# Optimization experiments

Hardware: AMD Instinct MI355X
Metric: run time of the kernel (lower is better)

## Reference

```python
import jax, jax.numpy as jnp
import numpy as np

N_NODES = 50000
N_EDGES = 800000
F_IN = 128
HEADS = 4
HEAD_DIM = 32  # hidden_size // heads
HIDDEN = HEADS * HEAD_DIM
N_GRAPHS = 64
LEAKY_SLOPE = 0.01
EPS_LN = 1e-5


def setup_inputs() -> dict:
    key = jax.random.key(0)
    ks = jax.random.split(key, 12)
    x = jax.random.normal(ks[0], (N_NODES, F_IN), dtype=jnp.float32)
    edge_index = jax.random.randint(ks[1], (2, N_EDGES), 0, N_NODES, dtype=jnp.int64)
    batch = jnp.sort(jax.random.randint(ks[2], (N_NODES,), 0, N_GRAPHS, dtype=jnp.int64))
    s = 1.0 / np.sqrt(F_IN).astype(np.float32)
    Wq = jax.random.normal(ks[3], (F_IN, HIDDEN), dtype=jnp.float32) * s
    bq = jnp.zeros((HIDDEN,), jnp.float32)
    Wk = jax.random.normal(ks[4], (F_IN, HIDDEN), dtype=jnp.float32) * s
    bk = jnp.zeros((HIDDEN,), jnp.float32)
    Wv = jax.random.normal(ks[5], (F_IN, HIDDEN), dtype=jnp.float32) * s
    bv = jnp.zeros((HIDDEN,), jnp.float32)
    Ws = jax.random.normal(ks[6], (F_IN, HIDDEN), dtype=jnp.float32) * s  # root/skip lin
    bs = jnp.zeros((HIDDEN,), jnp.float32)
    ln_w = jnp.ones((HIDDEN,), jnp.float32)
    ln_b = jnp.zeros((HIDDEN,), jnp.float32)
    return {"x": x, "edge_index": edge_index, "batch": batch,
            "Wq": Wq, "bq": bq, "Wk": Wk, "bk": bk, "Wv": Wv, "bv": bv,
            "Ws": Ws, "bs": bs, "ln_w": ln_w, "ln_b": ln_b}


def reference(x, edge_index, batch, Wq, bq, Wk, bk, Wv, bv, Ws, bs, ln_w, ln_b):
    N = x.shape[0]
    src, dst = edge_index[0], edge_index[1]  # message j(src) -> i(dst)
    q = (x @ Wq + bq).reshape(N, HEADS, HEAD_DIM)
    k = (x @ Wk + bk).reshape(N, HEADS, HEAD_DIM)
    v = (x @ Wv + bv).reshape(N, HEADS, HEAD_DIM)
    # per-edge attention logits [E, H]
    alpha = jnp.einsum('ehc,ehc->eh', q[dst], k[src]) / jnp.sqrt(jnp.float32(HEAD_DIM))
    # scatter-softmax over incoming edges of each destination node
    m = jax.ops.segment_max(alpha, dst, num_segments=N)
    m = jnp.where(jnp.isfinite(m), m, 0.0)  # empty segments -> -inf; neutralize
    ex = jnp.exp(alpha - m[dst])
    denom = jax.ops.segment_sum(ex, dst, num_segments=N)
    attn = ex / (denom[dst] + 1e-16)
    # scatter-add aggregation of weighted values, concat heads
    out = jax.ops.segment_sum(attn[:, :, None] * v[src], dst, num_segments=N)
    out = out.reshape(N, HIDDEN) + x @ Ws + bs  # root/skip connection
    # PyG graph-mode LayerNorm: normalize over all nodes+channels of each graph
    cnt = jax.ops.segment_sum(jnp.ones((N,), out.dtype), batch, num_segments=N_GRAPHS)
    norm = jnp.maximum(cnt, 1.0) * HIDDEN
    mean = jax.ops.segment_sum(out.sum(-1), batch, num_segments=N_GRAPHS) / norm
    outc = out - mean[batch][:, None]
    var = jax.ops.segment_sum((outc * outc).sum(-1), batch, num_segments=N_GRAPHS) / norm
    y = outc / jnp.sqrt(var + EPS_LN)[batch][:, None]
    y = y * ln_w + ln_b
    y = jnp.where(y > 0, y, LEAKY_SLOPE * y)  # LeakyReLU
    return (y, attn)
```

## Files before the change

kernel.cpp:

```cpp
#include <hip/hip_runtime.h>
#include <hip/hip_fp16.h>

constexpr int N_NODES = 50000;
constexpr int N_EDGES = 800000;
constexpr int HIDDEN  = 128;
constexpr float RSQRT_D = 0.17677669529663687f;
constexpr int Y_SIZE = N_NODES * HIDDEN;
constexpr int M_PAD  = 50048;
constexpr int SCAN_BLOCKS = 196;

constexpr size_t OFF_Q      = 0;
constexpr size_t OFF_K      = 6400000;
constexpr size_t OFF_V      = 12800000;
constexpr size_t OFF_S      = 19200000;
constexpr size_t OFF_DENOM  = 25600000;
constexpr size_t OFF_GSUM   = 25800000;
constexpr size_t OFF_GVAR   = 25800064;
constexpr size_t OFF_GCNT   = 25800128;
constexpr size_t OFF_DEG    = 25800192;
constexpr size_t OFF_OFFS   = 25850192;
constexpr size_t OFF_CURSOR = 25900224;
constexpr size_t OFF_CSRSRC = 25950224;
constexpr size_t OFF_CSREID = 26750224;
constexpr size_t OFF_PART   = 27550224;

typedef __attribute__((ext_vector_type(8))) short bf16x8;
typedef __attribute__((ext_vector_type(4))) float f32x4;

__device__ __forceinline__ short f2bf(float f) {
    unsigned u = __float_as_uint(f);
    unsigned r = (u + 0x7fff + ((u >> 16) & 1)) >> 16;
    return (short)r;
}

__device__ __forceinline__ void gload_lds16(const void* g, void* l) {
    __builtin_amdgcn_global_load_lds(
        (const __attribute__((address_space(1))) void*)g,
        (__attribute__((address_space(3))) void*)l, 16, 0, 0);
}

__global__ __launch_bounds__(256) void k_cvt_x(const float* __restrict__ x,
                                               short* __restrict__ xs)
{
    int tid = blockIdx.x * 256 + threadIdx.x;
    int row = tid >> 4, ci = tid & 15;
    short o[8];
    if (row < N_NODES) {
        float4 a = *(const float4*)&x[(size_t)row * 128 + ci * 8];
        float4 b = *(const float4*)&x[(size_t)row * 128 + ci * 8 + 4];
        o[0] = f2bf(a.x); o[1] = f2bf(a.y); o[2] = f2bf(a.z); o[3] = f2bf(a.w);
        o[4] = f2bf(b.x); o[5] = f2bf(b.y); o[6] = f2bf(b.z); o[7] = f2bf(b.w);
    } else {
        #pragma unroll
        for (int j = 0; j < 8; ++j) o[j] = 0;
    }
    int cs = ci ^ (row & 7);
    *(int4*)&xs[(size_t)row * 128 + cs * 8] = *(int4*)o;
}

__global__ __launch_bounds__(256) void k_cvt_w(
    const float* __restrict__ Wq, const float* __restrict__ Wk,
    const float* __restrict__ Wv, const float* __restrict__ Wsm,
    short* __restrict__ wt)
{
    int tid = blockIdx.x * 256 + threadIdx.x;
    int mat = tid >> 11, n = (tid >> 4) & 127, kg = tid & 15;
    const float* W = (mat == 0) ? Wq : (mat == 1) ? Wk : (mat == 2) ? Wv : Wsm;
    short o[8];
    #pragma unroll
    for (int j = 0; j < 8; ++j) o[j] = f2bf(W[(kg * 8 + j) * 128 + n]);
    int cs = kg ^ (n & 7);
    *(int4*)&wt[mat * 16384 + n * 128 + cs * 8] = *(int4*)o;
}

__global__ __launch_bounds__(256) void k_mm(
    const short* __restrict__ xs, const short* __restrict__ wt,
    const float* __restrict__ bq, const float* __restrict__ bk,
    const float* __restrict__ bv, const float* __restrict__ bs,
    float* __restrict__ q, __half* __restrict__ kb,
    __half* __restrict__ vb, float* __restrict__ s)
{
    __shared__ __align__(16) char As[32768];
    __shared__ __align__(16) char Bs[32768];
    const int t = threadIdx.x, lane = t & 63, wv = t >> 6;
    const int bm = blockIdx.x >> 2, nt = blockIdx.x & 3;
    const int m0 = bm * 128;

    const char* gA = (const char*)xs + (size_t)m0 * 256;
    const char* gB = (const char*)wt + nt * 32768;
    #pragma unroll
    for (int i = 0; i < 8; ++i) {
        int chunk = wv * 8 + i;
        gload_lds16(gA + chunk * 1024 + lane * 16, As + chunk * 1024);
        gload_lds16(gB + chunk * 1024 + lane * 16, Bs + chunk * 1024);
    }

    const float* Bb = (nt == 0) ? bq : (nt == 1) ? bk : (nt == 2) ? bv : bs;
    const int wm = wv >> 1, wn = wv & 1;
    f32x4 acc[4][4];
    #pragma unroll
    for (int nf = 0; nf < 4; ++nf) {
        float bc = Bb[wn * 64 + nf * 16 + (lane & 15)];
        #pragma unroll
        for (int mf = 0; mf < 4; ++mf) acc[mf][nf] = (f32x4){bc, bc, bc, bc};
    }
    __syncthreads();

    #pragma unroll
    for (int ks = 0; ks < 4; ++ks) {
        bf16x8 af[4], bfr[4];
        const int cbase = ks * 64 + ((lane >> 4) << 4);
        #pragma unroll
        for (int mf = 0; mf < 4; ++mf) {
            int mr = wm * 64 + mf * 16 + (lane & 15);
            af[mf] = *(const bf16x8*)(As + mr * 256 + (cbase ^ ((mr & 7) << 4)));
        }
        #pragma unroll
        for (int nf = 0; nf < 4; ++nf) {
            int nc = wn * 64 + nf * 16 + (lane & 15);
            bfr[nf] = *(const bf16x8*)(Bs + nc * 256 + (cbase ^ ((nc & 7) << 4)));
        }
        #pragma unroll
        for (int mf = 0; mf < 4; ++mf)
            #pragma unroll
            for (int nf = 0; nf < 4; ++nf)
                acc[mf][nf] = __builtin_amdgcn_mfma_f32_16x16x32_bf16(
                    af[mf], bfr[nf], acc[mf][nf], 0, 0, 0);
    }

    const int colbase = wn * 64 + (lane & 15);
    if (nt == 0 || nt == 3) {
        float* O = (nt == 0) ? q : s;
        #pragma unroll
        for (int mf = 0; mf < 4; ++mf) {
            int rowb = m0 + wm * 64 + mf * 16 + ((lane >> 4) << 2);
            #pragma unroll
            for (int nf = 0; nf < 4; ++nf) {
                int col = colbase + nf * 16;
                #pragma unroll
                for (int r = 0; r < 4; ++r) {
                    int node = rowb + r;
                    if (node < N_NODES) O[(size_t)node * 128 + col] = acc[mf][nf][r];
                }
            }
        }
    } else {
        __half* O = (nt == 1) ? kb : vb;
        #pragma unroll
        for (int mf = 0; mf < 4; ++mf) {
            int rowb = m0 + wm * 64 + mf * 16 + ((lane >> 4) << 2);
            #pragma unroll
            for (int nf = 0; nf < 4; ++nf) {
                int col = colbase + nf * 16;
                #pragma unroll
                for (int r = 0; r < 4; ++r) {
                    int node = rowb + r;
                    if (node < N_NODES)
                        O[(size_t)node * 128 + col] = __float2half_rn(acc[mf][nf][r]);
                }
            }
        }
    }
}

__global__ __launch_bounds__(256) void k_hist(const int* __restrict__ dst,
                                              int* __restrict__ deg)
{
    int e = blockIdx.x * 256 + threadIdx.x;
    atomicAdd(&deg[dst[e]], 1);
}

__global__ __launch_bounds__(256) void k_scan1(const int* __restrict__ deg,
                                               int* __restrict__ part)
{
    const int t = threadIdx.x;
    int idx = blockIdx.x * 256 + t;
    int v = (idx < N_NODES) ? deg[idx] : 0;
    #pragma unroll
    for (int o = 1; o < 64; o <<= 1) v += __shfl_xor(v, o);
    __shared__ int wsum[4];
    if ((t & 63) == 0) wsum[t >> 6] = v;
    __syncthreads();
    if (t == 0) part[blockIdx.x] = wsum[0] + wsum[1] + wsum[2] + wsum[3];
}

__global__ __launch_bounds__(256) void k_scan2(int* __restrict__ part)
{
    __shared__ int buf[256];
    const int t = threadIdx.x;
    int v = (t < SCAN_BLOCKS) ? part[t] : 0;
    buf[t] = v;
    __syncthreads();
    for (int o = 1; o < 256; o <<= 1) {
        int tmp = (t >= o) ? buf[t - o] : 0;
        __syncthreads();
        buf[t] += tmp;
        __syncthreads();
    }
    if (t < SCAN_BLOCKS) part[t] = buf[t] - v;
}

__global__ __launch_bounds__(256) void k_scan3(const int* __restrict__ deg,
                                               const int* __restrict__ part,
                                               int* __restrict__ offs,
                                               int* __restrict__ cursor)
{
    const int t = threadIdx.x;
    const int idx = blockIdx.x * 256 + t;
    const int lane = t & 63, w = t >> 6;
    int v = (idx < N_NODES) ? deg[idx] : 0;
    int inc = v;
    #pragma unroll
    for (int o = 1; o < 64; o <<= 1) {
        int nb = __shfl_up(inc, o);
        if (lane >= o) inc += nb;
    }
    __shared__ int wsum[4];
    if (lane == 63) wsum[w] = inc;
    __syncthreads();
    int wbase = 0;
    #pragma unroll
    for (int i = 0; i < 4; ++i) if (i < w) wbase += wsum[i];
    int excl = part[blockIdx.x] + wbase + inc - v;
    if (idx < N_NODES) {
        offs[idx] = excl;
        cursor[idx] = excl;
    }
    if (idx == 0) offs[N_NODES] = N_EDGES;
}

__global__ __launch_bounds__(256) void k_scatter(
    const int* __restrict__ src, const int* __restrict__ dst,
    int* __restrict__ cursor, int* __restrict__ csr_src, int* __restrict__ csr_eid)
{
    int e = blockIdx.x * 256 + threadIdx.x;
    int d = dst[e];
    int pos = atomicAdd(&cursor[d], 1);
    csr_src[pos] = src[e];
    csr_eid[pos] = e;
}

__global__ __launch_bounds__(256) void k_fused(
    const float* __restrict__ q, const __half2* __restrict__ kb,
    const __half2* __restrict__ vb, const float* __restrict__ s,
    const int* __restrict__ offs, const int* __restrict__ csr_src,
    const int* __restrict__ csr_eid,
    float* __restrict__ exbuf, float* __restrict__ denom,
    float* __restrict__ outb)
{
    const int t = threadIdx.x;
    const int lane = t & 63;
    const int n = blockIdx.x * 4 + (t >> 6);
    const int begin = offs[n], end = offs[n + 1];
    const float2 qv = *(const float2*)&q[(size_t)n * 128 + lane * 2];
    const int h = lane >> 4;
    float acc0 = 0.f, acc1 = 0.f, dsum = 0.f;
    int i = begin;
    for (; i + 4 <= end; i += 4) {
        int sn[4], eid[4];
        #pragma unroll
        for (int u = 0; u < 4; ++u) { sn[u] = csr_src[i + u]; eid[u] = csr_eid[i + u]; }
        __half2 kh[4], vh[4];
        #pragma unroll
        for (int u = 0; u < 4; ++u) kh[u] = kb[(size_t)sn[u] * 64 + lane];
        #pragma unroll
        for (int u = 0; u < 4; ++u) vh[u] = vb[(size_t)sn[u] * 64 + lane];
        float p[4];
        #pragma unroll
        for (int u = 0; u < 4; ++u) {
            float2 kf = __half22float2(kh[u]);
            p[u] = qv.x * kf.x + qv.y * kf.y;
        }
        #pragma unroll
        for (int u = 0; u < 4; ++u) p[u] += __shfl_xor(p[u], 1);
        #pragma unroll
        for (int u = 0; u < 4; ++u) p[u] += __shfl_xor(p[u], 2);
        #pragma unroll
        for (int u = 0; u < 4; ++u) p[u] += __shfl_xor(p[u], 4);
        #pragma unroll
        for (int u = 0; u < 4; ++u) p[u] += __shfl_xor(p[u], 8);
        #pragma unroll
        for (int u = 0; u < 4; ++u) {
            float ex = __expf(p[u] * RSQRT_D);
            dsum += ex;
            float2 vf = __half22float2(vh[u]);
            acc0 += ex * vf.x;
            acc1 += ex * vf.y;
            if ((lane & 15) == 0) exbuf[eid[u] * 4 + h] = ex;
        }
    }
    for (; i < end; ++i) {
        const int sn0 = csr_src[i];
        const int e0  = csr_eid[i];
        const __half2 kh0 = kb[(size_t)sn0 * 64 + lane];
        const __half2 vh0 = vb[(size_t)sn0 * 64 + lane];
        const float2 k0 = __half22float2(kh0);
        float p0 = qv.x * k0.x + qv.y * k0.y;
        p0 += __shfl_xor(p0, 1);
        p0 += __shfl_xor(p0, 2);
        p0 += __shfl_xor(p0, 4);
        p0 += __shfl_xor(p0, 8);
        const float ex0 = __expf(p0 * RSQRT_D);
        dsum += ex0;
        const float2 v0 = __half22float2(vh0);
        acc0 += ex0 * v0.x;
        acc1 += ex0 * v0.y;
        if ((lane & 15) == 0) exbuf[e0 * 4 + h] = ex0;
    }
    if ((lane & 15) == 0) denom[n * 4 + h] = dsum;
    const float rdn = 1.f / (dsum + 1e-16f);
    const float2 sv = *(const float2*)&s[(size_t)n * 128 + lane * 2];
    float2 o = make_float2(acc0 * rdn + sv.x, acc1 * rdn + sv.y);
    *(float2*)&outb[(size_t)n * 128 + lane * 2] = o;
}

__global__ __launch_bounds__(256) void k_norm(
    float* __restrict__ attn, const float* __restrict__ denom,
    const int* __restrict__ dst)
{
    int idx = blockIdx.x * 256 + threadIdx.x;
    int e = idx >> 2, h = idx & 3;
    attn[idx] = attn[idx] / (denom[dst[e] * 4 + h] + 1e-16f);
}

__global__ __launch_bounds__(256) void k_sum(
    const float* __restrict__ out, const int* __restrict__ batch,
    float* __restrict__ gsum, int* __restrict__ gcnt)
{
    __shared__ float nsum[32];
    __shared__ int   ngr[32];
    const int t = threadIdx.x;
    const int nl = t >> 3, part = t & 7;
    const int n = blockIdx.x * 32 + nl;
    float lsum = 0.f;
    if (n < N_NODES) {
        size_t base = (size_t)n * 128 + part * 16;
        #pragma unroll
        for (int i = 0; i < 4; ++i) {
            float4 o = *(const float4*)&out[base + i * 4];
            lsum += o.x + o.y + o.z + o.w;
        }
    }
    lsum += __shfl_xor(lsum, 1);
    lsum += __shfl_xor(lsum, 2);
    lsum += __shfl_xor(lsum, 4);
    if (part == 0) { nsum[nl] = lsum; ngr[nl] = (n < N_NODES) ? batch[n] : -1; }
    __syncthreads();
    if (t == 0) {
        float acc = 0.f; int cg = ngr[0], cnt = 0;
        for (int i = 0; i < 32; ++i) {
            int g = ngr[i];
            if (g != cg) {
                if (cg >= 0) { atomicAdd(&gsum[cg], acc); atomicAdd(&gcnt[cg], cnt); }
                acc = 0.f; cnt = 0; cg = g;
            }
            acc += nsum[i]; ++cnt;
        }
        if (cg >= 0) { atomicAdd(&gsum[cg], acc); atomicAdd(&gcnt[cg], cnt); }
    }
}

__global__ __launch_bounds__(256) void k_var(
    const float* __restrict__ out, const int* __restrict__ batch,
    const float* __restrict__ gsum, const int* __restrict__ gcnt,
    float* __restrict__ gvar)
{
    __shared__ float nsum[32];
    __shared__ int   ngr[32];
    const int t = threadIdx.x;
    const int nl = t >> 3, part = t & 7;
    const int n = blockIdx.x * 32 + nl;
    float lsum = 0.f;
    if (n < N_NODES) {
        int g = batch[n];
        float mean = gsum[g] / (fmaxf((float)gcnt[g], 1.f) * 128.f);
        size_t base = (size_t)n * 128 + part * 16;
        #pragma unroll
        for (int i = 0; i < 4; ++i) {
            float4 o = *(const float4*)&out[base + i * 4];
            float dx = o.x - mean, dy = o.y - mean, dz = o.z - mean, dw = o.w - mean;
            lsum += dx * dx + dy * dy + dz * dz + dw * dw;
        }
    }
    lsum += __shfl_xor(lsum, 1);
    lsum += __shfl_xor(lsum, 2);
    lsum += __shfl_xor(lsum, 4);
    if (part == 0) { nsum[nl] = lsum; ngr[nl] = (n < N_NODES) ? batch[n] : -1; }
    __syncthreads();
    if (t == 0) {
        float acc = 0.f; int cg = ngr[0];
        for (int i = 0; i < 32; ++i) {
            int g = ngr[i];
            if (g != cg) {
                if (cg >= 0) atomicAdd(&gvar[cg], acc);
                acc = 0.f; cg = g;
            }
            acc += nsum[i];
        }
        if (cg >= 0) atomicAdd(&gvar[cg], acc);
    }
}

__global__ __launch_bounds__(256) void k_final(
    const float* __restrict__ out, const int* __restrict__ batch,
    const float* __restrict__ gsum, const float* __restrict__ gvar,
    const int* __restrict__ gcnt,
    const float* __restrict__ lnw, const float* __restrict__ lnb,
    float* __restrict__ y)
{
    int idx = blockIdx.x * 256 + threadIdx.x;
    int n = idx >> 7, c = idx & 127;
    int g = batch[n];
    float norm = fmaxf((float)gcnt[g], 1.f) * 128.f;
    float mean = gsum[g] / norm;
    float var  = gvar[g] / norm;
    float inv  = rsqrtf(var + 1e-5f);
    float val  = (out[idx] - mean) * inv * lnw[c] + lnb[c];
    y[idx] = val > 0.f ? val : 0.01f * val;
}

extern "C" void kernel_launch(void* const* d_in, const int* in_sizes, int n_in,
                              void* d_out, int out_size, void* d_ws, size_t ws_size,
                              hipStream_t stream)
{
    (void)in_sizes; (void)n_in; (void)out_size; (void)ws_size;
    const float* x    = (const float*)d_in[0];
    const int*   ei   = (const int*)  d_in[1];
    const int*   batch= (const int*)  d_in[2];
    const float* Wq   = (const float*)d_in[3];
    const float* bq   = (const float*)d_in[4];
    const float* Wk   = (const float*)d_in[5];
    const float* bk   = (const float*)d_in[6];
    const float* Wv   = (const float*)d_in[7];
    const float* bv   = (const float*)d_in[8];
    const float* Wsm  = (const float*)d_in[9];
    const float* bs   = (const float*)d_in[10];
    const float* lnw  = (const float*)d_in[11];
    const float* lnb  = (const float*)d_in[12];

    float* outp = (float*)d_out;
    float* ws   = (float*)d_ws;

    const int* srcI = ei;
    const int* dstI = ei + N_EDGES;

    float*  q       = ws + OFF_Q;
    __half* kb      = (__half*)(ws + OFF_K);
    __half* vb      = (__half*)(ws + OFF_V);
    float*  s       = ws + OFF_S;
    float*  denom   = ws + OFF_DENOM;
    short*  wt      = (short*)(ws + OFF_DENOM);
    float*  gsum    = ws + OFF_GSUM;
    float*  gvar    = ws + OFF_GVAR;
    int*    gcnt    = (int*)(ws + OFF_GCNT);
    int*    deg     = (int*)(ws + OFF_DEG);
    int*    offs    = (int*)(ws + OFF_OFFS);
    int*    cursor  = (int*)(ws + OFF_CURSOR);
    int*    csr_src = (int*)(ws + OFF_CSRSRC);
    int*    csr_eid = (int*)(ws + OFF_CSREID);
    int*    partArr = (int*)(ws + OFF_PART);

    float* outb  = outp;
    short* x_swz = (short*)outp;
    float* attn  = outp + Y_SIZE;

    hipMemsetAsync(gsum, 0, (size_t)(192 + N_NODES) * sizeof(float), stream);

    k_cvt_w<<<32, 256, 0, stream>>>(Wq, Wk, Wv, Wsm, wt);
    k_cvt_x<<<(M_PAD * 16) / 256, 256, 0, stream>>>(x, x_swz);
    k_mm<<<(M_PAD / 128) * 4, 256, 0, stream>>>(x_swz, wt, bq, bk, bv, bs,
                                                q, kb, vb, s);

    k_hist<<<N_EDGES / 256, 256, 0, stream>>>(dstI, deg);
    k_scan1<<<SCAN_BLOCKS, 256, 0, stream>>>(deg, partArr);
    k_scan2<<<1, 256, 0, stream>>>(partArr);
    k_scan3<<<SCAN_BLOCKS, 256, 0, stream>>>(deg, partArr, offs, cursor);
    k_scatter<<<N_EDGES / 256, 256, 0, stream>>>(srcI, dstI, cursor, csr_src, csr_eid);
    k_fused<<<N_NODES / 4, 256, 0, stream>>>(q, (const __half2*)kb, (const __half2*)vb,
                                             s, offs, csr_src, csr_eid,
                                             attn, denom, outb);
    k_norm<<<(N_EDGES * 4) / 256, 256, 0, stream>>>(attn, denom, dstI);
    k_sum<<<(N_NODES + 31) / 32, 256, 0, stream>>>(outb, batch, gsum, gcnt);
    k_var<<<(N_NODES + 31) / 32, 256, 0, stream>>>(outb, batch, gsum, gcnt, gvar);
    k_final<<<Y_SIZE / 256, 256, 0, stream>>>(outb, batch, gsum, gvar, gcnt,
                                              lnw, lnb, outp);
}
```

Before: 272.6 us.

## Fuse conversions, compute all projections per tile, pack CSR, single-pass LN stats

Merges the x and W conversion kernels into one launch. The GEMM now loads each A tile once and loops over all four weight matrices, reloading B into shared memory between them, and q is stored as fp16. CSR source and edge-id arrays become one interleaved int2 array, and the gather loop is unrolled to 8 edges. The separate sum and variance passes are replaced by one pass that accumulates sum and sum of squares, computing variance as E[x^2]-mean^2, which risks cancellation error.

```diff
diff --git a/kernel.cpp b/kernel.cpp
--- a/kernel.cpp
+++ b/kernel.cpp
@@ -8,6 +8,7 @@
 constexpr int Y_SIZE = N_NODES * HIDDEN;
 constexpr int M_PAD  = 50048;
 constexpr int SCAN_BLOCKS = 196;
+constexpr int XCVT_BLOCKS = (M_PAD * 16) / 256;
 
 constexpr size_t OFF_Q      = 0;
 constexpr size_t OFF_K      = 6400000;
@@ -15,13 +16,12 @@
 constexpr size_t OFF_S      = 19200000;
 constexpr size_t OFF_DENOM  = 25600000;
 constexpr size_t OFF_GSUM   = 25800000;
-constexpr size_t OFF_GVAR   = 25800064;
+constexpr size_t OFF_GSQ    = 25800064;
 constexpr size_t OFF_GCNT   = 25800128;
 constexpr size_t OFF_DEG    = 25800192;
 constexpr size_t OFF_OFFS   = 25850192;
 constexpr size_t OFF_CURSOR = 25900224;
-constexpr size_t OFF_CSRSRC = 25950224;
-constexpr size_t OFF_CSREID = 26750224;
+constexpr size_t OFF_CSR    = 25950224;
 constexpr size_t OFF_PART   = 27550224;
 
 typedef __attribute__((ext_vector_type(8))) short bf16x8;
@@ -39,127 +39,141 @@
         (__attribute__((address_space(3))) void*)l, 16, 0, 0);
 }
 
-__global__ __launch_bounds__(256) void k_cvt_x(const float* __restrict__ x,
-                                               short* __restrict__ xs)
-{
-    int tid = blockIdx.x * 256 + threadIdx.x;
-    int row = tid >> 4, ci = tid & 15;
-    short o[8];
-    if (row < N_NODES) {
-        float4 a = *(const float4*)&x[(size_t)row * 128 + ci * 8];
-        float4 b = *(const float4*)&x[(size_t)row * 128 + ci * 8 + 4];
-        o[0] = f2bf(a.x); o[1] = f2bf(a.y); o[2] = f2bf(a.z); o[3] = f2bf(a.w);
-        o[4] = f2bf(b.x); o[5] = f2bf(b.y); o[6] = f2bf(b.z); o[7] = f2bf(b.w);
-    } else {
-        #pragma unroll
-        for (int j = 0; j < 8; ++j) o[j] = 0;
-    }
-    int cs = ci ^ (row & 7);
-    *(int4*)&xs[(size_t)row * 128 + cs * 8] = *(int4*)o;
-}
-
-__global__ __launch_bounds__(256) void k_cvt_w(
+__global__ __launch_bounds__(256) void k_cvt(
+    const float* __restrict__ x,
     const float* __restrict__ Wq, const float* __restrict__ Wk,
     const float* __restrict__ Wv, const float* __restrict__ Wsm,
-    short* __restrict__ wt)
-{
-    int tid = blockIdx.x * 256 + threadIdx.x;
-    int mat = tid >> 11, n = (tid >> 4) & 127, kg = tid & 15;
-    const float* W = (mat == 0) ? Wq : (mat == 1) ? Wk : (mat == 2) ? Wv : Wsm;
-    short o[8];
-    #pragma unroll
-    for (int j = 0; j < 8; ++j) o[j] = f2bf(W[(kg * 8 + j) * 128 + n]);
-    int cs = kg ^ (n & 7);
-    *(int4*)&wt[mat * 16384 + n * 128 + cs * 8] = *(int4*)o;
+    short* __restrict__ xs, short* __restrict__ wt)
+{
+    int b = blockIdx.x;
+    if (b < XCVT_BLOCKS) {
+        int tid = b * 256 + threadIdx.x;
+        int row = tid >> 4, ci = tid & 15;
+        short o[8];
+        if (row < N_NODES) {
+            float4 a = *(const float4*)&x[(size_t)row * 128 + ci * 8];
+            float4 bb = *(const float4*)&x[(size_t)row * 128 + ci * 8 + 4];
+            o[0] = f2bf(a.x); o[1] = f2bf(a.y); o[2] = f2bf(a.z); o[3] = f2bf(a.w);
+            o[4] = f2bf(bb.x); o[5] = f2bf(bb.y); o[6] = f2bf(bb.z); o[7] = f2bf(bb.w);
+        } else {
+            #pragma unroll
+            for (int j = 0; j < 8; ++j) o[j] = 0;
+        }
+        int cs = ci ^ (row & 7);
+        *(int4*)&xs[(size_t)row * 128 + cs * 8] = *(int4*)o;
+    } else {
+        int tid = (b - XCVT_BLOCKS) * 256 + threadIdx.x;
+        int mat = tid >> 11, n = (tid >> 4) & 127, kg = tid & 15;
+        const float* W = (mat == 0) ? Wq : (mat == 1) ? Wk : (mat == 2) ? Wv : Wsm;
+        short o[8];
+        #pragma unroll
+        for (int j = 0; j < 8; ++j) o[j] = f2bf(W[(kg * 8 + j) * 128 + n]);
+        int cs = kg ^ (n & 7);
+        *(int4*)&wt[mat * 16384 + n * 128 + cs * 8] = *(int4*)o;
+    }
 }
 
 __global__ __launch_bounds__(256) void k_mm(
     const short* __restrict__ xs, const short* __restrict__ wt,
     const float* __restrict__ bq, const float* __restrict__ bk,
     const float* __restrict__ bv, const float* __restrict__ bs,
-    float* __restrict__ q, __half* __restrict__ kb,
+    __half* __restrict__ q, __half* __restrict__ kb,
     __half* __restrict__ vb, float* __restrict__ s)
 {
     __shared__ __align__(16) char As[32768];
     __shared__ __align__(16) char Bs[32768];
     const int t = threadIdx.x, lane = t & 63, wv = t >> 6;
-    const int bm = blockIdx.x >> 2, nt = blockIdx.x & 3;
-    const int m0 = bm * 128;
+    const int m0 = blockIdx.x * 128;
+    const int wm = wv >> 1, wn = wv & 1;
 
     const char* gA = (const char*)xs + (size_t)m0 * 256;
-    const char* gB = (const char*)wt + nt * 32768;
     #pragma unroll
     for (int i = 0; i < 8; ++i) {
         int chunk = wv * 8 + i;
         gload_lds16(gA + chunk * 1024 + lane * 16, As + chunk * 1024);
-        gload_lds16(gB + chunk * 1024 + lane * 16, Bs + chunk * 1024);
-    }
-
-    const float* Bb = (nt == 0) ? bq : (nt == 1) ? bk : (nt == 2) ? bv : bs;
-    const int wm = wv >> 1, wn = wv & 1;
-    f32x4 acc[4][4];
-    #pragma unroll
-    for (int nf = 0; nf < 4; ++nf) {
-        float bc = Bb[wn * 64 + nf * 16 + (lane & 15)];
-        #pragma unroll
-        for (int mf = 0; mf < 4; ++mf) acc[mf][nf] = (f32x4){bc, bc, bc, bc};
+        gload_lds16((const char*)wt + chunk * 1024 + lane * 16, Bs + chunk * 1024);
     }
     __syncthreads();
 
+    bf16x8 af[4][4];
     #pragma unroll
     for (int ks = 0; ks < 4; ++ks) {
-        bf16x8 af[4], bfr[4];
         const int cbase = ks * 64 + ((lane >> 4) << 4);
         #pragma unroll
         for (int mf = 0; mf < 4; ++mf) {
             int mr = wm * 64 + mf * 16 + (lane & 15);
-            af[mf] = *(const bf16x8*)(As + mr * 256 + (cbase ^ ((mr & 7) << 4)));
-        }
+            af[ks][mf] = *(const bf16x8*)(As + mr * 256 + (cbase ^ ((mr & 7) << 4)));
+        }
+    }
+
+    const float* Bbs[4] = {bq, bk, bv, bs};
+    #pragma unroll
+    for (int mat = 0; mat < 4; ++mat) {
+        f32x4 acc[4][4];
         #pragma unroll
         for (int nf = 0; nf < 4; ++nf) {
-            int nc = wn * 64 + nf * 16 + (lane & 15);
-            bfr[nf] = *(const bf16x8*)(Bs + nc * 256 + (cbase ^ ((nc & 7) << 4)));
-        }
-        #pragma unroll
-        for (int mf = 0; mf < 4; ++mf)
-            #pragma unroll
-            for (int nf = 0; nf < 4; ++nf)
-                acc[mf][nf] = __builtin_amdgcn_mfma_f32_16x16x32_bf16(
-                    af[mf], bfr[nf], acc[mf][nf], 0, 0, 0);
-    }
-
-    const int colbase = wn * 64 + (lane & 15);
-    if (nt == 0 || nt == 3) {
-        float* O = (nt == 0) ? q : s;
-        #pragma unroll
-        for (int mf = 0; mf < 4; ++mf) {
-            int rowb = m0 + wm * 64 + mf * 16 + ((lane >> 4) << 2);
+            float bc = Bbs[mat][wn * 64 + nf * 16 + (lane & 15)];
+            #pragma unroll
+            for (int mf = 0; mf < 4; ++mf) acc[mf][nf] = (f32x4){bc, bc, bc, bc};
+        }
+        #pragma unroll
+        for (int ks = 0; ks < 4; ++ks) {
+            bf16x8 bfr[4];
+            const int cbase = ks * 64 + ((lane >> 4) << 4);
             #pragma unroll
             for (int nf = 0; nf < 4; ++nf) {
-                int col = colbase + nf * 16;
+                int nc = wn * 64 + nf * 16 + (lane & 15);
+                bfr[nf] = *(const bf16x8*)(Bs + nc * 256 + (cbase ^ ((nc & 7) << 4)));
+            }
+            #pragma unroll
+            for (int mf = 0; mf < 4; ++mf)
                 #pragma unroll
-                for (int r = 0; r < 4; ++r) {
-                    int node = rowb + r;
-                    if (node < N_NODES) O[(size_t)node * 128 + col] = acc[mf][nf][r];
+                for (int nf = 0; nf < 4; ++nf)
+                    acc[mf][nf] = __builtin_amdgcn_mfma_f32_16x16x32_bf16(
+                        af[ks][mf], bfr[nf], acc[mf][nf], 0, 0, 0);
+        }
+        __syncthreads();
+        if (mat < 3) {
+            const char* gB = (const char*)wt + (mat + 1) * 32768;
+            #pragma unroll
+            for (int i = 0; i < 8; ++i) {
+                int chunk = wv * 8 + i;
+                gload_lds16(gB + chunk * 1024 + lane * 16, Bs + chunk * 1024);
+            }
+        }
+        const int colbase = wn * 64 + (lane & 15);
+        if (mat == 3) {
+            #pragma unroll
+            for (int mf = 0; mf < 4; ++mf) {
+                int rowb = m0 + wm * 64 + mf * 16 + ((lane >> 4) << 2);
+                #pragma unroll
+                for (int nf = 0; nf < 4; ++nf) {
+                    int col = colbase + nf * 16;
+                    #pragma unroll
+                    for (int r = 0; r < 4; ++r) {
+                        int node = rowb + r;
+                        if (node < N_NODES) s[(size_t)node * 128 + col] = acc[mf][nf][r];
+                    }
                 }
             }
-        }
-    } else {
-        __half* O = (nt == 1) ? kb : vb;
-        #pragma unroll
-        for (int mf = 0; mf < 4; ++mf) {
-            int rowb = m0 + wm * 64 + mf * 16 + ((lane >> 4) << 2);
-            #pragma unroll
-            for (int nf = 0; nf < 4; ++nf) {
-                int col = colbase + nf * 16;
+        } else {
+            __half* O = (mat == 0) ? q : (mat == 1) ? kb : vb;
+            #pragma unroll
+            for (int mf = 0; mf < 4; ++mf) {
+                int rowb = m0 + wm * 64 + mf * 16 + ((lane >> 4) << 2);
                 #pragma unroll
-                for (int r = 0; r < 4; ++r) {
-                    int node = rowb + r;
-                    if (node < N_NODES)
-                        O[(size_t)node * 128 + col] = __float2half_rn(acc[mf][nf][r]);
+                for (int nf = 0; nf < 4; ++nf) {
+                    int col = colbase + nf * 16;
+                    #pragma unroll
+                    for (int r = 0; r < 4; ++r) {
+                        int node = rowb + r;
+                        if (node < N_NODES)
+                            O[(size_t)node * 128 + col] = __float2half_rn(acc[mf][nf][r]);
+                    }
                 }
             }
         }
+        __syncthreads();
     }
 }
 
@@ -231,20 +245,18 @@
 
 __global__ __launch_bounds__(256) void k_scatter(
     const int* __restrict__ src, const int* __restrict__ dst,
-    int* __restrict__ cursor, int* __restrict__ csr_src, int* __restrict__ csr_eid)
+    int* __restrict__ cursor, int2* __restrict__ csr)
 {
     int e = blockIdx.x * 256 + threadIdx.x;
     int d = dst[e];
     int pos = atomicAdd(&cursor[d], 1);
-    csr_src[pos] = src[e];
-    csr_eid[pos] = e;
+    csr[pos] = make_int2(src[e], e);
 }
 
 __global__ __launch_bounds__(256) void k_fused(
-    const float* __restrict__ q, const __half2* __restrict__ kb,
+    const __half2* __restrict__ qb, const __half2* __restrict__ kb,
     const __half2* __restrict__ vb, const float* __restrict__ s,
-    const int* __restrict__ offs, const int* __restrict__ csr_src,
-    const int* __restrict__ csr_eid,
+    const int* __restrict__ offs, const int2* __restrict__ csr,
     float* __restrict__ exbuf, float* __restrict__ denom,
     float* __restrict__ outb)
 {
@@ -252,48 +264,48 @@
     const int lane = t & 63;
     const int n = blockIdx.x * 4 + (t >> 6);
     const int begin = offs[n], end = offs[n + 1];
-    const float2 qv = *(const float2*)&q[(size_t)n * 128 + lane * 2];
+    const float2 qv = __half22float2(qb[(size_t)n * 64 + lane]);
+    const float2 sv = *(const float2*)&s[(size_t)n * 128 + lane * 2];
     const int h = lane >> 4;
     float acc0 = 0.f, acc1 = 0.f, dsum = 0.f;
     int i = begin;
-    for (; i + 4 <= end; i += 4) {
-        int sn[4], eid[4];
-        #pragma unroll
-        for (int u = 0; u < 4; ++u) { sn[u] = csr_src[i + u]; eid[u] = csr_eid[i + u]; }
-        __half2 kh[4], vh[4];
-        #pragma unroll
-        for (int u = 0; u < 4; ++u) kh[u] = kb[(size_t)sn[u] * 64 + lane];
-        #pragma unroll
-        for (int u = 0; u < 4; ++u) vh[u] = vb[(size_t)sn[u] * 64 + lane];
-        float p[4];
-        #pragma unroll
-        for (int u = 0; u < 4; ++u) {
+    for (; i + 8 <= end; i += 8) {
+        int2 c[8];
+        #pragma unroll
+        for (int u = 0; u < 8; ++u) c[u] = csr[i + u];
+        __half2 kh[8], vh[8];
+        #pragma unroll
+        for (int u = 0; u < 8; ++u) kh[u] = kb[(size_t)c[u].x * 64 + lane];
+        #pragma unroll
+        for (int u = 0; u < 8; ++u) vh[u] = vb[(size_t)c[u].x * 64 + lane];
+        float p[8];
+        #pragma unroll
+        for (int u = 0; u < 8; ++u) {
             float2 kf = __half22float2(kh[u]);
             p[u] = qv.x * kf.x + qv.y * kf.y;
         }
         #pragma unroll
-        for (int u = 0; u < 4; ++u) p[u] += __shfl_xor(p[u], 1);
-        #pragma unroll
-        for (int u = 0; u < 4; ++u) p[u] += __shfl_xor(p[u], 2);
-        #pragma unroll
-        for (int u = 0; u < 4; ++u) p[u] += __shfl_xor(p[u], 4);
-        #pragma unroll
-        for (int u = 0; u < 4; ++u) p[u] += __shfl_xor(p[u], 8);
-        #pragma unroll
-        for (int u = 0; u < 4; ++u) {
+        for (int u = 0; u < 8; ++u) p[u] += __shfl_xor(p[u], 1);
+        #pragma unroll
+        for (int u = 0; u < 8; ++u) p[u] += __shfl_xor(p[u], 2);
+        #pragma unroll
+        for (int u = 0; u < 8; ++u) p[u] += __shfl_xor(p[u], 4);
+        #pragma unroll
+        for (int u = 0; u < 8; ++u) p[u] += __shfl_xor(p[u], 8);
+        #pragma unroll
+        for (int u = 0; u < 8; ++u) {
             float ex = __expf(p[u] * RSQRT_D);
             dsum += ex;
             float2 vf = __half22float2(vh[u]);
             acc0 += ex * vf.x;
             acc1 += ex * vf.y;
-            if ((lane & 15) == 0) exbuf[eid[u] * 4 + h] = ex;
+            if ((lane & 15) == 0) exbuf[c[u].y * 4 + h] = ex;
         }
     }
     for (; i < end; ++i) {
-        const int sn0 = csr_src[i];
-        const int e0  = csr_eid[i];
-        const __half2 kh0 = kb[(size_t)sn0 * 64 + lane];
-        const __half2 vh0 = vb[(size_t)sn0 * 64 + lane];
+        const int2 c0 = csr[i];
+        const __half2 kh0 = kb[(size_t)c0.x * 64 + lane];
+        const __half2 vh0 = vb[(size_t)c0.x * 64 + lane];
         const float2 k0 = __half22float2(kh0);
         float p0 = qv.x * k0.x + qv.y * k0.y;
         p0 += __shfl_xor(p0, 1);
@@ -305,11 +317,10 @@
         const float2 v0 = __half22float2(vh0);
         acc0 += ex0 * v0.x;
         acc1 += ex0 * v0.y;
-        if ((lane & 15) == 0) exbuf[e0 * 4 + h] = ex0;
+        if ((lane & 15) == 0) exbuf[c0.y * 4 + h] = ex0;
     }
     if ((lane & 15) == 0) denom[n * 4 + h] = dsum;
     const float rdn = 1.f / (dsum + 1e-16f);
-    const float2 sv = *(const float2*)&s[(size_t)n * 128 + lane * 2];
     float2 o = make_float2(acc0 * rdn + sv.x, acc1 * rdn + sv.y);
     *(float2*)&outb[(size_t)n * 128 + lane * 2] = o;
 }
@@ -323,87 +334,51 @@
     attn[idx] = attn[idx] / (denom[dst[e] * 4 + h] + 1e-16f);
 }
 
-__global__ __launch_bounds__(256) void k_sum(
+__global__ __launch_bounds__(256) void k_stats(
     const float* __restrict__ out, const int* __restrict__ batch,
-    float* __restrict__ gsum, int* __restrict__ gcnt)
-{
-    __shared__ float nsum[32];
+    float* __restrict__ gsum, float* __restrict__ gsq, int* __restrict__ gcnt)
+{
+    __shared__ float nsum[32], nsq[32];
     __shared__ int   ngr[32];
     const int t = threadIdx.x;
     const int nl = t >> 3, part = t & 7;
     const int n = blockIdx.x * 32 + nl;
-    float lsum = 0.f;
+    float lsum = 0.f, lsq = 0.f;
     if (n < N_NODES) {
         size_t base = (size_t)n * 128 + part * 16;
         #pragma unroll
         for (int i = 0; i < 4; ++i) {
             float4 o = *(const float4*)&out[base + i * 4];
             lsum += o.x + o.y + o.z + o.w;
-        }
-    }
-    lsum += __shfl_xor(lsum, 1);
-    lsum += __shfl_xor(lsum, 2);
-    lsum += __shfl_xor(lsum, 4);
-    if (part == 0) { nsum[nl] = lsum; ngr[nl] = (n < N_NODES) ? batch[n] : -1; }
+            lsq  += o.x * o.x + o.y * o.y + o.z * o.z + o.w * o.w;
+        }
+    }
+    #pragma unroll
+    for (int o = 1; o < 8; o <<= 1) {
+        lsum += __shfl_xor(lsum, o);
+        lsq  += __shfl_xor(lsq, o);
+    }
+    if (part == 0) { nsum[nl] = lsum; nsq[nl] = lsq; ngr[nl] = (n < N_NODES) ? batch[n] : -1; }
     __syncthreads();
     if (t == 0) {
-        float acc = 0.f; int cg = ngr[0], cnt = 0;
+        float acc = 0.f, accq = 0.f; int cg = ngr[0], cnt = 0;
         for (int i = 0; i < 32; ++i) {
             int g = ngr[i];
             if (g != cg) {
-                if (cg >= 0) { atomicAdd(&gsum[cg], acc); atomicAdd(&gcnt[cg], cnt); }
-                acc = 0.f; cnt = 0; cg = g;
+                if (cg >= 0) { atomicAdd(&gsum[cg], acc); atomicAdd(&gsq[cg], accq);
+                               atomicAdd(&gcnt[cg], cnt); }
+                acc = 0.f; accq = 0.f; cnt = 0; cg = g;
             }
-            acc += nsum[i]; ++cnt;
-        }
-        if (cg >= 0) { atomicAdd(&gsum[cg], acc); atomicAdd(&gcnt[cg], cnt); }
-    }
-}
-
-__global__ __launch_bounds__(256) void k_var(
-    const float* __restrict__ out, const int* __restrict__ batch,
-    const float* __restrict__ gsum, const int* __restrict__ gcnt,
-    float* __restrict__ gvar)
-{
-    __shared__ float nsum[32];
-    __shared__ int   ngr[32];
-    const int t = threadIdx.x;
-    const int nl = t >> 3, part = t & 7;
-    const int n = blockIdx.x * 32 + nl;
-    float lsum = 0.f;
-    if (n < N_NODES) {
-        int g = batch[n];
-        float mean = gsum[g] / (fmaxf((float)gcnt[g], 1.f) * 128.f);
-        size_t base = (size_t)n * 128 + part * 16;
-        #pragma unroll
-        for (int i = 0; i < 4; ++i) {
-            float4 o = *(const float4*)&out[base + i * 4];
-            float dx = o.x - mean, dy = o.y - mean, dz = o.z - mean, dw = o.w - mean;
-            lsum += dx * dx + dy * dy + dz * dz + dw * dw;
-        }
-    }
-    lsum += __shfl_xor(lsum, 1);
-    lsum += __shfl_xor(lsum, 2);
-    lsum += __shfl_xor(lsum, 4);
-    if (part == 0) { nsum[nl] = lsum; ngr[nl] = (n < N_NODES) ? batch[n] : -1; }
-    __syncthreads();
-    if (t == 0) {
-        float acc = 0.f; int cg = ngr[0];
-        for (int i = 0; i < 32; ++i) {
-            int g = ngr[i];
-            if (g != cg) {
-                if (cg >= 0) atomicAdd(&gvar[cg], acc);
-                acc = 0.f; cg = g;
-            }
-            acc += nsum[i];
-        }
-        if (cg >= 0) atomicAdd(&gvar[cg], acc);
+            acc += nsum[i]; accq += nsq[i]; ++cnt;
+        }
+        if (cg >= 0) { atomicAdd(&gsum[cg], acc); atomicAdd(&gsq[cg], accq);
+                       atomicAdd(&gcnt[cg], cnt); }
     }
 }
 
 __global__ __launch_bounds__(256) void k_final(
     const float* __restrict__ out, const int* __restrict__ batch,
-    const float* __restrict__ gsum, const float* __restrict__ gvar,
+    const float* __restrict__ gsum, const float* __restrict__ gsq,
     const int* __restrict__ gcnt,
     const float* __restrict__ lnw, const float* __restrict__ lnb,
     float* __restrict__ y)
@@ -413,7 +388,7 @@
     int g = batch[n];
     float norm = fmaxf((float)gcnt[g], 1.f) * 128.f;
     float mean = gsum[g] / norm;
-    float var  = gvar[g] / norm;
+    float var  = gsq[g] / norm - mean * mean;
     float inv  = rsqrtf(var + 1e-5f);
     float val  = (out[idx] - mean) * inv * lnw[c] + lnb[c];
     y[idx] = val > 0.f ? val : 0.01f * val;
@@ -444,20 +419,19 @@
     const int* srcI = ei;
     const int* dstI = ei + N_EDGES;
 
-    float*  q       = ws + OFF_Q;
+    __half* qb      = (__half*)(ws + OFF_Q);
     __half* kb      = (__half*)(ws + OFF_K);
     __half* vb      = (__half*)(ws + OFF_V);
     float*  s       = ws + OFF_S;
     float*  denom   = ws + OFF_DENOM;
     short*  wt      = (short*)(ws + OFF_DENOM);
     float*  gsum    = ws + OFF_GSUM;
-    float*  gvar    = ws + OFF_GVAR;
+    float*  gsq     = ws + OFF_GSQ;
     int*    gcnt    = (int*)(ws + OFF_GCNT);
     int*    deg     = (int*)(ws + OFF_DEG);
     int*    offs    = (int*)(ws + OFF_OFFS);
     int*    cursor  = (int*)(ws + OFF_CURSOR);
-    int*    csr_src = (int*)(ws + OFF_CSRSRC);
-    int*    csr_eid = (int*)(ws + OFF_CSREID);
+    int2*   csr     = (int2*)(ws + OFF_CSR);
     int*    partArr = (int*)(ws + OFF_PART);
 
     float* outb  = outp;
@@ -466,22 +440,19 @@
 
     hipMemsetAsync(gsum, 0, (size_t)(192 + N_NODES) * sizeof(float), stream);
 
-    k_cvt_w<<<32, 256, 0, stream>>>(Wq, Wk, Wv, Wsm, wt);
-    k_cvt_x<<<(M_PAD * 16) / 256, 256, 0, stream>>>(x, x_swz);
-    k_mm<<<(M_PAD / 128) * 4, 256, 0, stream>>>(x_swz, wt, bq, bk, bv, bs,
-                                                q, kb, vb, s);
+    k_cvt<<<XCVT_BLOCKS + 32, 256, 0, stream>>>(x, Wq, Wk, Wv, Wsm, x_swz, wt);
+    k_mm<<<M_PAD / 128, 256, 0, stream>>>(x_swz, wt, bq, bk, bv, bs, qb, kb, vb, s);
 
     k_hist<<<N_EDGES / 256, 256, 0, stream>>>(dstI, deg);
     k_scan1<<<SCAN_BLOCKS, 256, 0, stream>>>(deg, partArr);
     k_scan2<<<1, 256, 0, stream>>>(partArr);
     k_scan3<<<SCAN_BLOCKS, 256, 0, stream>>>(deg, partArr, offs, cursor);
-    k_scatter<<<N_EDGES / 256, 256, 0, stream>>>(srcI, dstI, cursor, csr_src, csr_eid);
-    k_fused<<<N_NODES / 4, 256, 0, stream>>>(q, (const __half2*)kb, (const __half2*)vb,
-                                             s, offs, csr_src, csr_eid,
+    k_scatter<<<N_EDGES / 256, 256, 0, stream>>>(srcI, dstI, cursor, csr);
+    k_fused<<<N_NODES / 4, 256, 0, stream>>>((const __half2*)qb, (const __half2*)kb,
+                                             (const __half2*)vb, s, offs, csr,
                                              attn, denom, outb);
     k_norm<<<(N_EDGES * 4) / 256, 256, 0, stream>>>(attn, denom, dstI);
-    k_sum<<<(N_NODES + 31) / 32, 256, 0, stream>>>(outb, batch, gsum, gcnt);
-    k_var<<<(N_NODES + 31) / 32, 256, 0, stream>>>(outb, batch, gsum, gcnt, gvar);
-    k_final<<<Y_SIZE / 256, 256, 0, stream>>>(outb, batch, gsum, gvar, gcnt,
+    k_stats<<<(N_NODES + 31) / 32, 256, 0, stream>>>(outb, batch, gsum, gsq, gcnt);
+    k_final<<<Y_SIZE / 256, 256, 0, stream>>>(outb, batch, gsum, gsq, gcnt,
                                               lnw, lnb, outp);
 }
```

Result: faster. 266.3 us (-2.3%).
